# Kernel tuning notes

Hardware: AMD Instinct MI355X
Metric: run time of the kernel (lower is better)

## Reference

```python
import jax, jax.numpy as jnp
import numpy as np

B, S, DM = 8, 1024, 1024
H, DH = 16, 64  # num_heads, per-head dim (q=k=v=r)
SCALE = 64 ** 1 / 2  # faithful to source: d_k**1/2 == d_k/2 == 32.0


def setup_inputs() -> dict:
    key = jax.random.key(0)
    ks = jax.random.split(key, 13)
    std = 1.0 / np.sqrt(DM)
    def lin(k):
        kw, kb = jax.random.split(k)
        W = jax.random.uniform(kw, (DM, H * DH), jnp.float32, -std, std)
        b = jax.random.uniform(kb, (H * DH,), jnp.float32, -std, std)
        return W, b
    Wq, bq = lin(ks[0]); Wk, bk = lin(ks[1]); Wv, bv = lin(ks[2]); Wr, br = lin(ks[3])
    Wo = jax.random.uniform(ks[4], (H * DH, DM), jnp.float32, -std, std)
    bo = jax.random.uniform(ks[5], (DM,), jnp.float32, -std, std)
    return {
        "value": jax.random.normal(ks[6], (B, S, DM), jnp.float32),
        "key": jax.random.normal(ks[7], (B, S, DM), jnp.float32),
        "query": jax.random.normal(ks[8], (B, S, DM), jnp.float32),
        "Wq": Wq, "bq": bq, "Wk": Wk, "bk": bk,
        "Wv": Wv, "bv": bv, "Wr": Wr, "br": br,
        "Wo": Wo, "bo": bo,
    }


def reference(value, key, query, Wq, bq, Wk, bk, Wv, bv, Wr, br, Wo, bo):
    b = query.shape[0]
    # projections -> [b, s, h, d] -> [b, h, s, d]
    q = (query @ Wq + bq).reshape(b, -1, H, DH).transpose(0, 2, 1, 3)
    k = (key @ Wk + bk).reshape(b, -1, H, DH).transpose(0, 2, 1, 3)
    v = (value @ Wv + bv).reshape(b, -1, H, DH).transpose(0, 2, 1, 3)
    r = (query @ Wr + br).reshape(b, -1, H, DH).transpose(0, 2, 1, 3)
    energy = jnp.einsum('bhid,bhjd->bhij', q, k)
    attn = jax.nn.softmax(energy / SCALE, axis=-1)
    ctx = jnp.einsum('bhjd,bhij->bhid', v, attn)
    gated = (ctx * r).transpose(0, 2, 1, 3)  # R-gating, back to [b, s, h, d]
    out = gated.reshape(b, -1, H * DH) @ Wo + bo
    return out
```

## Files before the change

kernel.cpp:

```cpp
#include <hip/hip_runtime.h>
#include <stdint.h>

#define B_ 8
#define S_ 1024
#define DM_ 1024
#define H_ 16
#define DH_ 64
#define M_ (B_*S_)

typedef unsigned short u16;
typedef unsigned int u32;
typedef __attribute__((ext_vector_type(8))) short bf16x8;
typedef __attribute__((ext_vector_type(4))) float f32x4;

__device__ __forceinline__ u16 f2bf(float f){
  union { float f; u32 u; } x; x.f = f;
  u32 r = x.u + 0x7fffu + ((x.u >> 16) & 1u);
  return (u16)(r >> 16);
}
__device__ __forceinline__ float bf2f(u16 u){
  union { u32 u; float f; } x; x.u = ((u32)u) << 16; return x.f;
}
__device__ __forceinline__ u32 cvtpk(float lo, float hi){
  u32 r; asm("v_cvt_pk_bf16_f32 %0, %1, %2" : "=v"(r) : "v"(lo), "v"(hi)); return r;
}
__device__ __forceinline__ void gload16(const void* g, void* l){
  __builtin_amdgcn_global_load_lds((const __attribute__((address_space(1))) void*)g,
                                   (__attribute__((address_space(3))) void*)l, 16, 0, 0);
}

__global__ void k_cvt_act(const float* __restrict__ v, const float* __restrict__ k,
                          const float* __restrict__ q, u16* __restrict__ vb,
                          u16* __restrict__ kb, u16* __restrict__ qb){
  int z = blockIdx.y;
  const float* src = (z == 0) ? v : (z == 1) ? k : q;
  u16* dst = (z == 0) ? vb : (z == 1) ? kb : qb;
  size_t i = ((size_t)blockIdx.x * blockDim.x + threadIdx.x) * 8;
  float4 a = *(const float4*)(src + i);
  float4 b = *(const float4*)(src + i + 4);
  uint4 o;
  o.x = (u32)f2bf(a.x) | ((u32)f2bf(a.y) << 16);
  o.y = (u32)f2bf(a.z) | ((u32)f2bf(a.w) << 16);
  o.z = (u32)f2bf(b.x) | ((u32)f2bf(b.y) << 16);
  o.w = (u32)f2bf(b.z) | ((u32)f2bf(b.w) << 16);
  *(uint4*)(dst + i) = o;
}

__global__ void k_cvt_wt(const float* __restrict__ w0, const float* __restrict__ w1,
                         const float* __restrict__ w2, const float* __restrict__ w3,
                         const float* __restrict__ w4,
                         u16* __restrict__ t0, u16* __restrict__ t1, u16* __restrict__ t2,
                         u16* __restrict__ t3, u16* __restrict__ t4){
  __shared__ float tile[32][33];
  int z = blockIdx.z;
  const float* src = (z==0)?w0:(z==1)?w1:(z==2)?w2:(z==3)?w3:w4;
  u16* dst = (z==0)?t0:(z==1)?t1:(z==2)?t2:(z==3)?t3:t4;
  int n0 = blockIdx.x * 32, k0 = blockIdx.y * 32;
  int tx = threadIdx.x, ty = threadIdx.y;
#pragma unroll
  for (int i=0;i<4;i++) tile[ty+8*i][tx] = src[(size_t)(k0+ty+8*i)*DM_ + n0+tx];
  __syncthreads();
#pragma unroll
  for (int i=0;i<4;i++) dst[(size_t)(n0+ty+8*i)*DM_ + k0+tx] = f2bf(tile[tx][ty+8*i]);
}

template<int OUTMODE>
__global__ __launch_bounds__(256) void k_gemm(const u16* __restrict__ A, const u16* __restrict__ Bt,
                                              const float* __restrict__ bias, void* __restrict__ Out){
  __shared__ u16 As[128*64];
  __shared__ u16 Bs[128*64];
  const int tid = threadIdx.x;
  const int w = tid >> 6, l = tid & 63, g = l >> 4, s = l & 15;
  const int wr = w >> 1, wc = w & 1;
  const int m0 = blockIdx.x << 7, n0 = blockIdx.y << 7;
  f32x4 acc[4][4];
#pragma unroll
  for (int i=0;i<4;i++)
#pragma unroll
    for (int j=0;j<4;j++) acc[i][j] = (f32x4){0.f,0.f,0.f,0.f};

  for (int k0 = 0; k0 < 1024; k0 += 64){
    __syncthreads();
#pragma unroll
    for (int i=0;i<4;i++){
      int c = tid + i*256;
      int m = c >> 3, slot = c & 7;
      gload16(A + ((size_t)(m0+m) << 10) + (k0 + ((slot ^ (m & 7)) << 3)),
              &As[(i*256 + w*64) * 8]);
    }
#pragma unroll
    for (int i=0;i<4;i++){
      int c = tid + i*256;
      int n = c >> 3, slot = c & 7;
      gload16(Bt + ((size_t)(n0+n) << 10) + (k0 + ((slot ^ (n & 7)) << 3)),
              &Bs[(i*256 + w*64) * 8]);
    }
    __syncthreads();
#pragma unroll
    for (int ks=0; ks<2; ks++){
      bf16x8 af[4], bfv[4];
#pragma unroll
      for (int mi=0;mi<4;mi++){
        int m = wr*64 + mi*16 + s;
        af[mi] = *(const bf16x8*)&As[m*64 + (((ks*4+g) ^ (s & 7)) << 3)];
      }
#pragma unroll
      for (int ni=0;ni<4;ni++){
        int n = wc*64 + ni*16 + s;
        bfv[ni] = *(const bf16x8*)&Bs[n*64 + (((ks*4+g) ^ (s & 7)) << 3)];
      }
#pragma unroll
      for (int mi=0;mi<4;mi++)
#pragma unroll
        for (int ni=0;ni<4;ni++)
          acc[mi][ni] = __builtin_amdgcn_mfma_f32_16x16x32_bf16(af[mi], bfv[ni], acc[mi][ni], 0, 0, 0);
    }
  }
#pragma unroll
  for (int ni=0;ni<4;ni++){
    int col = n0 + wc*64 + ni*16 + s;
    float bv = bias[col];
#pragma unroll
    for (int mi=0;mi<4;mi++){
      int row = m0 + wr*64 + mi*16 + g*4;
      if (OUTMODE == 2){
        union { short4 v; u16 e[4]; } pk;
#pragma unroll
        for (int r=0;r<4;r++) pk.e[r] = f2bf(acc[mi][ni][r] + bv);
        size_t vrow = ((size_t)(row >> 10) * 16 + (col >> 6)) * 64 + (col & 63);
        *(short4*)&((u16*)Out)[(vrow << 10) + (row & 1023)] = pk.v;
      } else {
#pragma unroll
        for (int r=0;r<4;r++){
          float val = acc[mi][ni][r] + bv;
          if (OUTMODE == 1)
            ((float*)Out)[((size_t)(row+r) << 10) + col] = val;
          else
            ((u16*)Out)[((size_t)(row+r) << 10) + col] = f2bf(val);
        }
      }
    }
  }
}

__global__ __launch_bounds__(256) void k_attn(const u16* __restrict__ qp, const u16* __restrict__ kp,
                                              const u16* __restrict__ vtg, const u16* __restrict__ rp,
                                              u16* __restrict__ gated){
  __shared__ u16 Ks[64*64];
  __shared__ u16 Vs[64*64];
  __shared__ u32 PsU[4*16*32];
  const int tid = threadIdx.x;
  const int w = tid >> 6, l = tid & 63, g = l >> 4, s = l & 15;
  const int q0 = blockIdx.x << 6;
  const int bh = blockIdx.y;
  const int b = bh >> 4, h = bh & 15;
  const size_t base = ((size_t)b << 20);
  const int colh = h << 6;
  const float KL = 1.4426950408889634f / 32.0f;

  const size_t qoff = base + ((size_t)(q0 + w*16 + s) << 10) + colh;
  bf16x8 qf0 = *(const bf16x8*)(qp + qoff + g*8);
  bf16x8 qf1 = *(const bf16x8*)(qp + qoff + 32 + g*8);
  const size_t vbase = ((size_t)(b*16 + h)) << 16;

  u32* PsW = PsU + (w << 9);
  const int sx2 = (s & 15) << 1;

  float mrun = -1e30f, lsum = 0.f;
  f32x4 of[4];
#pragma unroll
  for (int d=0;d<4;d++) of[d] = (f32x4){0.f,0.f,0.f,0.f};

  for (int kv0 = 0; kv0 < S_; kv0 += 64){
    __syncthreads();
#pragma unroll
    for (int i=0;i<2;i++){
      int c = tid + i*256;
      int sj = c >> 3, slot = c & 7;
      gload16(kp + base + ((size_t)(kv0+sj) << 10) + colh + ((slot ^ (sj & 7)) << 3),
              &Ks[(i*256 + w*64) * 8]);
    }
#pragma unroll
    for (int i=0;i<2;i++){
      int c = tid + i*256;
      int d = c >> 3, slot = c & 7;
      gload16(vtg + vbase + ((size_t)d << 10) + kv0 + ((slot ^ (d & 7)) << 3),
              &Vs[(i*256 + w*64) * 8]);
    }
    __syncthreads();

    f32x4 e2[4];
#pragma unroll
    for (int sjf=0;sjf<4;sjf++){
      e2[sjf] = (f32x4){0.f,0.f,0.f,0.f};
      int sj = sjf*16 + s;
      bf16x8 kf0 = *(const bf16x8*)&Ks[sj*64 + ((g ^ (s & 7)) << 3)];
      e2[sjf] = __builtin_amdgcn_mfma_f32_16x16x32_bf16(kf0, qf0, e2[sjf], 0, 0, 0);
      bf16x8 kf1 = *(const bf16x8*)&Ks[sj*64 + (((4+g) ^ (s & 7)) << 3)];
      e2[sjf] = __builtin_amdgcn_mfma_f32_16x16x32_bf16(kf1, qf1, e2[sjf], 0, 0, 0);
    }
    float rm = fmaxf(fmaxf(fmaxf(e2[0][0], e2[0][1]), fmaxf(e2[0][2], e2[0][3])),
                     fmaxf(fmaxf(e2[1][0], e2[1][1]), fmaxf(e2[1][2], e2[1][3])));
    rm = fmaxf(rm, fmaxf(fmaxf(fmaxf(e2[2][0], e2[2][1]), fmaxf(e2[2][2], e2[2][3])),
                         fmaxf(fmaxf(e2[3][0], e2[3][1]), fmaxf(e2[3][2], e2[3][3]))));
    rm = fmaxf(rm, __shfl_xor(rm, 16, 64));
    rm = fmaxf(rm, __shfl_xor(rm, 32, 64));
    float nm = fmaxf(mrun, rm);
    float alpha = __builtin_amdgcn_exp2f((mrun - nm) * KL);
    mrun = nm;
    lsum *= alpha;
    float ac[4];
#pragma unroll
    for (int r=0;r<4;r++) ac[r] = __shfl(alpha, g*4 + r, 64);
#pragma unroll
    for (int d=0; d<4; d++)
#pragma unroll
      for (int r=0;r<4;r++) of[d][r] *= ac[r];

    const float mk = mrun * KL;
#pragma unroll
    for (int sjf=0;sjf<4;sjf++){
      float p0 = __builtin_amdgcn_exp2f(e2[sjf][0]*KL - mk);
      float p1 = __builtin_amdgcn_exp2f(e2[sjf][1]*KL - mk);
      float p2 = __builtin_amdgcn_exp2f(e2[sjf][2]*KL - mk);
      float p3 = __builtin_amdgcn_exp2f(e2[sjf][3]*KL - mk);
      lsum += (p0 + p1) + (p2 + p3);
      uint2 pk; pk.x = cvtpk(p0, p1); pk.y = cvtpk(p2, p3);
      int phys = (8*sjf + 2*g) ^ sx2;
      *reinterpret_cast<uint2*>(&PsW[(s << 5) + phys]) = pk;
    }
    union { u32 u[4]; bf16x8 v; } pa0, pa1;
    {
      uint2 r0 = *reinterpret_cast<const uint2*>(&PsW[(s << 5) + ((4*g    ) ^ sx2)]);
      uint2 r1 = *reinterpret_cast<const uint2*>(&PsW[(s << 5) + ((4*g + 2) ^ sx2)]);
      pa0.u[0] = r0.x; pa0.u[1] = r0.y; pa0.u[2] = r1.x; pa0.u[3] = r1.y;
      uint2 r2 = *reinterpret_cast<const uint2*>(&PsW[(s << 5) + ((16 + 4*g    ) ^ sx2)]);
      uint2 r3 = *reinterpret_cast<const uint2*>(&PsW[(s << 5) + ((16 + 4*g + 2) ^ sx2)]);
      pa1.u[0] = r2.x; pa1.u[1] = r2.y; pa1.u[2] = r3.x; pa1.u[3] = r3.y;
    }
#pragma unroll
    for (int df=0; df<4; df++){
      int d = df*16 + s;
      bf16x8 v0 = *(const bf16x8*)&Vs[d*64 + ((g ^ (s & 7)) << 3)];
      bf16x8 v1 = *(const bf16x8*)&Vs[d*64 + (((4+g) ^ (s & 7)) << 3)];
      of[df] = __builtin_amdgcn_mfma_f32_16x16x32_bf16(pa0.v, v0, of[df], 0, 0, 0);
      of[df] = __builtin_amdgcn_mfma_f32_16x16x32_bf16(pa1.v, v1, of[df], 0, 0, 0);
    }
  }
  lsum += __shfl_xor(lsum, 16, 64);
  lsum += __shfl_xor(lsum, 32, 64);
  float inv = 1.0f / lsum;
  float ic[4];
#pragma unroll
  for (int r=0;r<4;r++) ic[r] = __shfl(inv, g*4 + r, 64);
#pragma unroll
  for (int df=0; df<4; df++){
#pragma unroll
    for (int r=0;r<4;r++){
      size_t row = (size_t)(q0 + w*16 + g*4 + r);
      size_t idx = base + (row << 10) + colh + df*16 + s;
      float o = of[df][r] * ic[r];
      float rg = bf2f(rp[idx]);
      gated[idx] = f2bf(o * rg);
    }
  }
}

extern "C" void kernel_launch(void* const* d_in, const int* in_sizes, int n_in,
                              void* d_out, int out_size, void* d_ws, size_t ws_size,
                              hipStream_t stream){
  (void)in_sizes; (void)n_in; (void)out_size; (void)ws_size;
  const float* value = (const float*)d_in[0];
  const float* key   = (const float*)d_in[1];
  const float* query = (const float*)d_in[2];
  const float* Wq = (const float*)d_in[3];  const float* bq = (const float*)d_in[4];
  const float* Wk = (const float*)d_in[5];  const float* bk = (const float*)d_in[6];
  const float* Wv = (const float*)d_in[7];  const float* bv = (const float*)d_in[8];
  const float* Wr = (const float*)d_in[9];  const float* br = (const float*)d_in[10];
  const float* Wo = (const float*)d_in[11]; const float* bo = (const float*)d_in[12];

  char* ws = (char*)d_ws;
  const size_t MB = (size_t)1 << 20;
  u16* qb  = (u16*)(ws + 0*MB);
  u16* kb  = (u16*)(ws + 16*MB);
  u16* vb  = (u16*)(ws + 32*MB);
  u16* wqt = (u16*)(ws + 48*MB);
  u16* wkt = (u16*)(ws + 50*MB);
  u16* wvt = (u16*)(ws + 52*MB);
  u16* wrt = (u16*)(ws + 54*MB);
  u16* wot = (u16*)(ws + 56*MB);
  u16* qpj = (u16*)(ws + 58*MB);
  u16* kpj = (u16*)(ws + 74*MB);
  u16* vtg = (u16*)(ws + 90*MB);
  u16* rpj = (u16*)(ws + 106*MB);
  u16* gat = qb;

  k_cvt_act<<<dim3(4096, 3), 256, 0, stream>>>(value, key, query, vb, kb, qb);
  k_cvt_wt<<<dim3(32, 32, 5), dim3(32, 8), 0, stream>>>(Wq, Wk, Wv, Wr, Wo,
                                                        wqt, wkt, wvt, wrt, wot);
  k_gemm<0><<<dim3(64, 8), 256, 0, stream>>>(qb, wqt, bq, qpj);
  k_gemm<0><<<dim3(64, 8), 256, 0, stream>>>(qb, wrt, br, rpj);
  k_gemm<0><<<dim3(64, 8), 256, 0, stream>>>(kb, wkt, bk, kpj);
  k_gemm<2><<<dim3(64, 8), 256, 0, stream>>>(vb, wvt, bv, vtg);
  k_attn<<<dim3(16, 128), 256, 0, stream>>>(qpj, kpj, vtg, rpj, gat);
  k_gemm<1><<<dim3(64, 8), 256, 0, stream>>>(gat, wot, bo, d_out);
}
```

Measured before the change: 224.1 us.

## Fuse projection GEMMs, double-buffer attention KV tiles, and add lazy softmax rescale

The four projection GEMMs are merged into one launch over a concatenated weight buffer, so a single grid of 2048 blocks covers Q, R, K and V. The attention kernel now double-buffers K/V tiles in shared memory so the next tile loads while the current one computes. Its block index is swizzled for cache locality, and the running-max rescale of the accumulator is skipped unless the max grows by more than a threshold. The lazy rescale changes numerics only slightly, and the extra shared-memory buffers may lower occupancy.

Result: faster. 210.2 us (-6.2%).

```diff
diff --git a/kernel.cpp b/kernel.cpp
--- a/kernel.cpp
+++ b/kernel.cpp
@@ -49,12 +49,11 @@
 __global__ void k_cvt_wt(const float* __restrict__ w0, const float* __restrict__ w1,
                          const float* __restrict__ w2, const float* __restrict__ w3,
                          const float* __restrict__ w4,
-                         u16* __restrict__ t0, u16* __restrict__ t1, u16* __restrict__ t2,
-                         u16* __restrict__ t3, u16* __restrict__ t4){
+                         u16* __restrict__ wall, u16* __restrict__ wot){
   __shared__ float tile[32][33];
   int z = blockIdx.z;
   const float* src = (z==0)?w0:(z==1)?w1:(z==2)?w2:(z==3)?w3:w4;
-  u16* dst = (z==0)?t0:(z==1)?t1:(z==2)?t2:(z==3)?t3:t4;
+  u16* dst = (z<4) ? (wall + (size_t)z * 1048576) : wot;
   int n0 = blockIdx.x * 32, k0 = blockIdx.y * 32;
   int tx = threadIdx.x, ty = threadIdx.y;
 #pragma unroll
@@ -64,9 +63,91 @@
   for (int i=0;i<4;i++) dst[(size_t)(n0+ty+8*i)*DM_ + k0+tx] = f2bf(tile[tx][ty+8*i]);
 }
 
-template<int OUTMODE>
-__global__ __launch_bounds__(256) void k_gemm(const u16* __restrict__ A, const u16* __restrict__ Bt,
-                                              const float* __restrict__ bias, void* __restrict__ Out){
+__global__ __launch_bounds__(256) void k_proj(const u16* __restrict__ qb, const u16* __restrict__ kb,
+                                              const u16* __restrict__ vb, const u16* __restrict__ wall,
+                                              const float* __restrict__ bqp, const float* __restrict__ brp,
+                                              const float* __restrict__ bkp, const float* __restrict__ bvp,
+                                              u16* __restrict__ qpj, u16* __restrict__ rpj,
+                                              u16* __restrict__ kpj, u16* __restrict__ vtg){
+  __shared__ u16 As[128*64];
+  __shared__ u16 Bs[128*64];
+  const int tid = threadIdx.x;
+  const int w = tid >> 6, l = tid & 63, g = l >> 4, s = l & 15;
+  const int wr = w >> 1, wc = w & 1;
+  const int m0 = blockIdx.x << 7;
+  const int ng0 = blockIdx.y << 7;
+  const int chunk = ng0 >> 10;
+  const u16* A = (chunk < 2) ? qb : (chunk == 2) ? kb : vb;
+  const float* bias = (chunk==0)?bqp:(chunk==1)?brp:(chunk==2)?bkp:bvp;
+  f32x4 acc[4][4];
+#pragma unroll
+  for (int i=0;i<4;i++)
+#pragma unroll
+    for (int j=0;j<4;j++) acc[i][j] = (f32x4){0.f,0.f,0.f,0.f};
+
+  for (int k0 = 0; k0 < 1024; k0 += 64){
+    __syncthreads();
+#pragma unroll
+    for (int i=0;i<4;i++){
+      int c = tid + i*256;
+      int m = c >> 3, slot = c & 7;
+      gload16(A + ((size_t)(m0+m) << 10) + (k0 + ((slot ^ (m & 7)) << 3)),
+              &As[(i*256 + w*64) * 8]);
+    }
+#pragma unroll
+    for (int i=0;i<4;i++){
+      int c = tid + i*256;
+      int n = c >> 3, slot = c & 7;
+      gload16(wall + ((size_t)(ng0+n) << 10) + (k0 + ((slot ^ (n & 7)) << 3)),
+              &Bs[(i*256 + w*64) * 8]);
+    }
+    __syncthreads();
+#pragma unroll
+    for (int ks=0; ks<2; ks++){
+      bf16x8 af[4], bfv[4];
+#pragma unroll
+      for (int mi=0;mi<4;mi++){
+        int m = wr*64 + mi*16 + s;
+        af[mi] = *(const bf16x8*)&As[m*64 + (((ks*4+g) ^ (s & 7)) << 3)];
+      }
+#pragma unroll
+      for (int ni=0;ni<4;ni++){
+        int n = wc*64 + ni*16 + s;
+        bfv[ni] = *(const bf16x8*)&Bs[n*64 + (((ks*4+g) ^ (s & 7)) << 3)];
+      }
+#pragma unroll
+      for (int mi=0;mi<4;mi++)
+#pragma unroll
+        for (int ni=0;ni<4;ni++)
+          acc[mi][ni] = __builtin_amdgcn_mfma_f32_16x16x32_bf16(af[mi], bfv[ni], acc[mi][ni], 0, 0, 0);
+    }
+  }
+  u16* outp = (chunk==0)?qpj:(chunk==1)?rpj:kpj;
+#pragma unroll
+  for (int ni=0;ni<4;ni++){
+    int cg = ng0 + wc*64 + ni*16 + s;
+    int col = cg & 1023;
+    float bv = bias[col];
+#pragma unroll
+    for (int mi=0;mi<4;mi++){
+      int row = m0 + wr*64 + mi*16 + g*4;
+      if (chunk == 3){
+        union { short4 v; u16 e[4]; } pk;
+#pragma unroll
+        for (int r=0;r<4;r++) pk.e[r] = f2bf(acc[mi][ni][r] + bv);
+        size_t vrow = ((size_t)(row >> 10) * 16 + (col >> 6)) * 64 + (col & 63);
+        *(short4*)&vtg[(vrow << 10) + (row & 1023)] = pk.v;
+      } else {
+#pragma unroll
+        for (int r=0;r<4;r++)
+          outp[((size_t)(row+r) << 10) + col] = f2bf(acc[mi][ni][r] + bv);
+      }
+    }
+  }
+}
+
+__global__ __launch_bounds__(256) void k_gemm_out(const u16* __restrict__ A, const u16* __restrict__ Bt,
+                                                  const float* __restrict__ bias, float* __restrict__ Out){
   __shared__ u16 As[128*64];
   __shared__ u16 Bs[128*64];
   const int tid = threadIdx.x;
@@ -123,22 +204,9 @@
 #pragma unroll
     for (int mi=0;mi<4;mi++){
       int row = m0 + wr*64 + mi*16 + g*4;
-      if (OUTMODE == 2){
-        union { short4 v; u16 e[4]; } pk;
-#pragma unroll
-        for (int r=0;r<4;r++) pk.e[r] = f2bf(acc[mi][ni][r] + bv);
-        size_t vrow = ((size_t)(row >> 10) * 16 + (col >> 6)) * 64 + (col & 63);
-        *(short4*)&((u16*)Out)[(vrow << 10) + (row & 1023)] = pk.v;
-      } else {
-#pragma unroll
-        for (int r=0;r<4;r++){
-          float val = acc[mi][ni][r] + bv;
-          if (OUTMODE == 1)
-            ((float*)Out)[((size_t)(row+r) << 10) + col] = val;
-          else
-            ((u16*)Out)[((size_t)(row+r) << 10) + col] = f2bf(val);
-        }
-      }
+#pragma unroll
+      for (int r=0;r<4;r++)
+        Out[((size_t)(row+r) << 10) + col] = acc[mi][ni][r] + bv;
     }
   }
 }
@@ -146,13 +214,15 @@
 __global__ __launch_bounds__(256) void k_attn(const u16* __restrict__ qp, const u16* __restrict__ kp,
                                               const u16* __restrict__ vtg, const u16* __restrict__ rp,
                                               u16* __restrict__ gated){
-  __shared__ u16 Ks[64*64];
-  __shared__ u16 Vs[64*64];
+  __shared__ u16 Ks[2][64*64];
+  __shared__ u16 Vs[2][64*64];
   __shared__ u32 PsU[4*16*32];
   const int tid = threadIdx.x;
   const int w = tid >> 6, l = tid & 63, g = l >> 4, s = l & 15;
-  const int q0 = blockIdx.x << 6;
-  const int bh = blockIdx.y;
+  const int bid = blockIdx.x;
+  const int swz = (bid & 7) * 256 + (bid >> 3);
+  const int q0 = (swz & 15) << 6;
+  const int bh = swz >> 4;
   const int b = bh >> 4, h = bh & 15;
   const size_t base = ((size_t)b << 20);
   const int colh = h << 6;
@@ -164,58 +234,72 @@
   const size_t vbase = ((size_t)(b*16 + h)) << 16;
 
   u32* PsW = PsU + (w << 9);
-  const int sx2 = (s & 15) << 1;
+  const int sx2 = s << 1;
 
   float mrun = -1e30f, lsum = 0.f;
   f32x4 of[4];
 #pragma unroll
   for (int d=0;d<4;d++) of[d] = (f32x4){0.f,0.f,0.f,0.f};
 
-  for (int kv0 = 0; kv0 < S_; kv0 += 64){
-    __syncthreads();
-#pragma unroll
-    for (int i=0;i<2;i++){
-      int c = tid + i*256;
-      int sj = c >> 3, slot = c & 7;
-      gload16(kp + base + ((size_t)(kv0+sj) << 10) + colh + ((slot ^ (sj & 7)) << 3),
-              &Ks[(i*256 + w*64) * 8]);
-    }
-#pragma unroll
-    for (int i=0;i<2;i++){
-      int c = tid + i*256;
-      int d = c >> 3, slot = c & 7;
-      gload16(vtg + vbase + ((size_t)d << 10) + kv0 + ((slot ^ (d & 7)) << 3),
-              &Vs[(i*256 + w*64) * 8]);
-    }
-    __syncthreads();
+#define STAGE_KV(BUF, KV0) do { \
+    _Pragma("unroll") \
+    for (int i=0;i<2;i++){ \
+      int c = tid + i*256; \
+      int sj = c >> 3, slot = c & 7; \
+      gload16(kp + base + ((size_t)((KV0)+sj) << 10) + colh + ((slot ^ (sj & 7)) << 3), \
+              &Ks[BUF][(i*256 + w*64) * 8]); \
+    } \
+    _Pragma("unroll") \
+    for (int i=0;i<2;i++){ \
+      int c = tid + i*256; \
+      int d = c >> 3, slot = c & 7; \
+      gload16(vtg + vbase + ((size_t)d << 10) + (KV0) + ((slot ^ (d & 7)) << 3), \
+              &Vs[BUF][(i*256 + w*64) * 8]); \
+    } \
+  } while(0)
+
+  STAGE_KV(0, 0);
+  __syncthreads();
+
+  int cur = 0;
+  for (int t = 0; t < 16; t++){
+    if (t < 15) STAGE_KV(cur ^ 1, (t+1) << 6);
+    const u16* ksb = Ks[cur];
+    const u16* vsb = Vs[cur];
 
     f32x4 e2[4];
 #pragma unroll
     for (int sjf=0;sjf<4;sjf++){
       e2[sjf] = (f32x4){0.f,0.f,0.f,0.f};
       int sj = sjf*16 + s;
-      bf16x8 kf0 = *(const bf16x8*)&Ks[sj*64 + ((g ^ (s & 7)) << 3)];
+      bf16x8 kf0 = *(const bf16x8*)&ksb[sj*64 + ((g ^ (s & 7)) << 3)];
       e2[sjf] = __builtin_amdgcn_mfma_f32_16x16x32_bf16(kf0, qf0, e2[sjf], 0, 0, 0);
-      bf16x8 kf1 = *(const bf16x8*)&Ks[sj*64 + (((4+g) ^ (s & 7)) << 3)];
+      bf16x8 kf1 = *(const bf16x8*)&ksb[sj*64 + (((4+g) ^ (s & 7)) << 3)];
       e2[sjf] = __builtin_amdgcn_mfma_f32_16x16x32_bf16(kf1, qf1, e2[sjf], 0, 0, 0);
     }
-    float rm = fmaxf(fmaxf(fmaxf(e2[0][0], e2[0][1]), fmaxf(e2[0][2], e2[0][3])),
-                     fmaxf(fmaxf(e2[1][0], e2[1][1]), fmaxf(e2[1][2], e2[1][3])));
-    rm = fmaxf(rm, fmaxf(fmaxf(fmaxf(e2[2][0], e2[2][1]), fmaxf(e2[2][2], e2[2][3])),
-                         fmaxf(fmaxf(e2[3][0], e2[3][1]), fmaxf(e2[3][2], e2[3][3]))));
+    float rm = fmaxf(fmaxf(e2[0][0], e2[0][1]), e2[0][2]);
+    rm = fmaxf(fmaxf(rm, e2[0][3]), e2[1][0]);
+    rm = fmaxf(fmaxf(rm, e2[1][1]), e2[1][2]);
+    rm = fmaxf(fmaxf(rm, e2[1][3]), e2[2][0]);
+    rm = fmaxf(fmaxf(rm, e2[2][1]), e2[2][2]);
+    rm = fmaxf(fmaxf(rm, e2[2][3]), e2[3][0]);
+    rm = fmaxf(fmaxf(rm, e2[3][1]), e2[3][2]);
+    rm = fmaxf(rm, e2[3][3]);
     rm = fmaxf(rm, __shfl_xor(rm, 16, 64));
     rm = fmaxf(rm, __shfl_xor(rm, 32, 64));
-    float nm = fmaxf(mrun, rm);
-    float alpha = __builtin_amdgcn_exp2f((mrun - nm) * KL);
-    mrun = nm;
-    lsum *= alpha;
-    float ac[4];
-#pragma unroll
-    for (int r=0;r<4;r++) ac[r] = __shfl(alpha, g*4 + r, 64);
-#pragma unroll
-    for (int d=0; d<4; d++)
-#pragma unroll
-      for (int r=0;r<4;r++) of[d][r] *= ac[r];
+    if (!__all(rm <= mrun + 177.0f)){
+      float nm = fmaxf(mrun, rm);
+      float alpha = __builtin_amdgcn_exp2f((mrun - nm) * KL);
+      mrun = nm;
+      lsum *= alpha;
+      float ac[4];
+#pragma unroll
+      for (int r=0;r<4;r++) ac[r] = __shfl(alpha, g*4 + r, 64);
+#pragma unroll
+      for (int d=0; d<4; d++)
+#pragma unroll
+        for (int r=0;r<4;r++) of[d][r] *= ac[r];
+    }
 
     const float mk = mrun * KL;
 #pragma unroll
@@ -241,12 +325,16 @@
 #pragma unroll
     for (int df=0; df<4; df++){
       int d = df*16 + s;
-      bf16x8 v0 = *(const bf16x8*)&Vs[d*64 + ((g ^ (s & 7)) << 3)];
-      bf16x8 v1 = *(const bf16x8*)&Vs[d*64 + (((4+g) ^ (s & 7)) << 3)];
+      bf16x8 v0 = *(const bf16x8*)&vsb[d*64 + ((g ^ (s & 7)) << 3)];
+      bf16x8 v1 = *(const bf16x8*)&vsb[d*64 + (((4+g) ^ (s & 7)) << 3)];
       of[df] = __builtin_amdgcn_mfma_f32_16x16x32_bf16(pa0.v, v0, of[df], 0, 0, 0);
       of[df] = __builtin_amdgcn_mfma_f32_16x16x32_bf16(pa1.v, v1, of[df], 0, 0, 0);
     }
-  }
+    __syncthreads();
+    cur ^= 1;
+  }
+#undef STAGE_KV
+
   lsum += __shfl_xor(lsum, 16, 64);
   lsum += __shfl_xor(lsum, 32, 64);
   float inv = 1.0f / lsum;
@@ -281,27 +369,21 @@
 
   char* ws = (char*)d_ws;
   const size_t MB = (size_t)1 << 20;
-  u16* qb  = (u16*)(ws + 0*MB);
-  u16* kb  = (u16*)(ws + 16*MB);
-  u16* vb  = (u16*)(ws + 32*MB);
-  u16* wqt = (u16*)(ws + 48*MB);
-  u16* wkt = (u16*)(ws + 50*MB);
-  u16* wvt = (u16*)(ws + 52*MB);
-  u16* wrt = (u16*)(ws + 54*MB);
-  u16* wot = (u16*)(ws + 56*MB);
-  u16* qpj = (u16*)(ws + 58*MB);
-  u16* kpj = (u16*)(ws + 74*MB);
-  u16* vtg = (u16*)(ws + 90*MB);
-  u16* rpj = (u16*)(ws + 106*MB);
-  u16* gat = qb;
+  u16* qb   = (u16*)(ws + 0*MB);
+  u16* kb   = (u16*)(ws + 16*MB);
+  u16* vb   = (u16*)(ws + 32*MB);
+  u16* wall = (u16*)(ws + 48*MB);
+  u16* wot  = (u16*)(ws + 56*MB);
+  u16* qpj  = (u16*)(ws + 58*MB);
+  u16* kpj  = (u16*)(ws + 74*MB);
+  u16* vtg  = (u16*)(ws + 90*MB);
+  u16* rpj  = (u16*)(ws + 106*MB);
+  u16* gat  = qb;
 
   k_cvt_act<<<dim3(4096, 3), 256, 0, stream>>>(value, key, query, vb, kb, qb);
-  k_cvt_wt<<<dim3(32, 32, 5), dim3(32, 8), 0, stream>>>(Wq, Wk, Wv, Wr, Wo,
-                                                        wqt, wkt, wvt, wrt, wot);
-  k_gemm<0><<<dim3(64, 8), 256, 0, stream>>>(qb, wqt, bq, qpj);
-  k_gemm<0><<<dim3(64, 8), 256, 0, stream>>>(qb, wrt, br, rpj);
-  k_gemm<0><<<dim3(64, 8), 256, 0, stream>>>(kb, wkt, bk, kpj);
-  k_gemm<2><<<dim3(64, 8), 256, 0, stream>>>(vb, wvt, bv, vtg);
-  k_attn<<<dim3(16, 128), 256, 0, stream>>>(qpj, kpj, vtg, rpj, gat);
-  k_gemm<1><<<dim3(64, 8), 256, 0, stream>>>(gat, wot, bo, d_out);
-}
+  k_cvt_wt<<<dim3(32, 32, 5), dim3(32, 8), 0, stream>>>(Wq, Wr, Wk, Wv, Wo, wall, wot);
+  k_proj<<<dim3(64, 32), 256, 0, stream>>>(qb, kb, vb, wall, bq, br, bk, bv,
+                                           qpj, rpj, kpj, vtg);
+  k_attn<<<2048, 256, 0, stream>>>(qpj, kpj, vtg, rpj, gat);
+  k_gemm_out<<<dim3(64, 8), 256, 0, stream>>>(gat, wot, bo, (float*)d_out);
+}
```
